# Performance work log

Measured on AMD Instinct MI355X. Metric: run time of the kernel, lower is better.

The kernel has to match this reference:

```python
import jax, jax.numpy as jnp
import numpy as np

N_Q = 9      # qubits -> state dim 512
N_L = 10     # circuit layers
DIM = 2 ** N_Q
B = 16384    # batch
N_CLS = 10


def _apply_1q(psi, U, q):
    # psi: [B, 2,...,2] (N_Q qubit axes); U: [2,2] complex
    psi = jnp.moveaxis(psi, q + 1, 1)
    shp = psi.shape
    psi = jnp.einsum('ij,bjk->bik', U, psi.reshape(shp[0], 2, -1)).reshape(shp)
    return jnp.moveaxis(psi, 1, q + 1)


def _apply_2q(psi, U, q0, q1):
    # U: [4,4] complex acting on (q0, q1)
    psi = jnp.moveaxis(psi, (q0 + 1, q1 + 1), (1, 2))
    shp = psi.shape
    psi = jnp.einsum('ij,bjk->bik', U, psi.reshape(shp[0], 4, -1)).reshape(shp)
    return jnp.moveaxis(psi, (1, 2), (q0 + 1, q1 + 1))


def _rot_mat(phi, theta, omega):
    # PennyLane Rot = RZ(omega) RY(theta) RZ(phi)
    c, s = jnp.cos(theta / 2), jnp.sin(theta / 2)
    a, b = (phi + omega) / 2, (phi - omega) / 2
    return jnp.stack([
        jnp.stack([jnp.exp(-1j * a) * c, -jnp.exp(1j * b) * s]),
        jnp.stack([jnp.exp(-1j * b) * s, jnp.exp(1j * a) * c]),
    ]).astype(jnp.complex64)


def _crx_mat(t):
    c, s = jnp.cos(t / 2), jnp.sin(t / 2)
    rx = jnp.stack([jnp.stack([c + 0j, -1j * s]),
                    jnp.stack([-1j * s, c + 0j])]).astype(jnp.complex64)
    return jnp.eye(4, dtype=jnp.complex64).at[2:, 2:].set(rx)


def _layer(psi, rot_n, crx_n):
    for i in range(N_Q):
        psi = _apply_1q(psi, _rot_mat(rot_n[i, 0], rot_n[i, 1], rot_n[i, 2]), i)
    for i in range(N_Q):
        psi = _apply_2q(psi, _crx_mat(crx_n[i, 0]), i, (i + 1) % N_Q)
    return psi


def _circuit(x, rot, crx):
    # AmplitudeEmbedding(normalize=True)
    psi = (x / jnp.linalg.norm(x, axis=1, keepdims=True)).astype(jnp.complex64)
    psi = psi.reshape((x.shape[0],) + (2,) * N_Q)
    for n in range(N_L):
        psi = _layer(psi, rot[n], crx[n])
    probs = psi.real ** 2 + psi.imag ** 2
    # <Z_q> = P(bit_q = 0) - P(bit_q = 1)
    zs = []
    for q in range(N_Q):
        axes = tuple(a for a in range(1, N_Q + 1) if a != q + 1)
        p = probs.sum(axis=axes)  # [B, 2]
        zs.append(p[:, 0] - p[:, 1])
    return jnp.stack(zs, axis=1)  # [B, N_Q]


def setup_inputs() -> dict:
    key = jax.random.key(0)
    k0, k1, k2, k3, k4 = jax.random.split(key, 5)
    x = jax.random.normal(k0, (B, DIM), jnp.float32)
    rot = jax.random.normal(k1, (N_L, N_Q, 3), jnp.float32)
    crx = jax.random.normal(k2, (N_L, N_Q, 1), jnp.float32)
    fc_w = jax.random.normal(k3, (N_CLS, N_Q), jnp.float32) * 0.3
    fc_b = jax.random.normal(k4, (N_CLS,), jnp.float32) * 0.1
    return {"x": x, "rot": rot, "crx": crx, "fc_w": fc_w, "fc_b": fc_b}


def reference(x, rot, crx, fc_w, fc_b):
    z = _circuit(x, rot, crx)          # [B, 9]
    logits = z @ fc_w.T + fc_b         # [B, 10]
    return jax.nn.log_softmax(logits, axis=1)
```

## Files before the change

kernel.cpp:

```cpp
#include <hip/hip_runtime.h>
#include <hip/hip_bf16.h>
#include <math.h>

#define NQ 9
#define NL 10
#define DIM 512
#define NCLS 10
#define B_TOT 16384

#define A_OFF   ((size_t)0)
#define BT_OFF  ((size_t)16 << 20)
#define C_OFF   ((size_t)32 << 20)
#define WS_NEED (((size_t)96) << 20)

__device__ __forceinline__ float shx(float v, int m) { return __shfl_xor(v, m, 64); }

__device__ __forceinline__ int looks_bf16(const void* p, int count) {
  const unsigned short* u = (const unsigned short*)p;
  int n = count < 64 ? count : 64;
  int good = 0;
  for (int i = 0; i < n; ++i) {
    unsigned short v = u[i];
    int e = (v >> 7) & 0xFF;
    good += (e >= 100 && e <= 140) || ((v & 0x7FFF) == 0);
  }
  return good * 8 >= n * 7;
}

__device__ __forceinline__ float ld(const void* p, int i, int isbf) {
  if (isbf) return __uint_as_float(((unsigned)((const unsigned short*)p)[i]) << 16);
  return ((const float*)p)[i];
}

template<int M>
__device__ __forceinline__ void rot_x(float (&sr)[8], float (&si)[8], const float* u) {
  float4 uA = *(const float4*)u;
  float4 uB = *(const float4*)(u + 4);
  bool hi = (threadIdx.x & M) != 0;
  float ar = hi ? uB.z : uA.x, ai = hi ? uB.w : uA.y;
  float br = hi ? uB.x : uA.z, bi = hi ? uB.y : uA.w;
#pragma unroll
  for (int r = 0; r < 8; ++r) {
    float pr = shx(sr[r], M), pi = shx(si[r], M);
    float nr = ar * sr[r] - ai * si[r] + br * pr - bi * pi;
    float ni = ar * si[r] + ai * sr[r] + br * pi + bi * pr;
    sr[r] = nr; si[r] = ni;
  }
}
template<int S>
__device__ __forceinline__ void rot_r(float (&sr)[8], float (&si)[8], const float* u) {
  float4 uA = *(const float4*)u;
  float4 uB = *(const float4*)(u + 4);
#pragma unroll
  for (int r0 = 0; r0 < 8; ++r0) {
    if (r0 & S) continue;
    int r1 = r0 + S;
    float a0r = sr[r0], a0i = si[r0], a1r = sr[r1], a1i = si[r1];
    sr[r0] = uA.x * a0r - uA.y * a0i + uA.z * a1r - uA.w * a1i;
    si[r0] = uA.x * a0i + uA.y * a0r + uA.z * a1i + uA.w * a1r;
    sr[r1] = uB.x * a0r - uB.y * a0i + uB.z * a1r - uB.w * a1i;
    si[r1] = uB.x * a0i + uB.y * a0r + uB.z * a1i + uB.w * a1r;
  }
}
template<int MC, int MT>
__device__ __forceinline__ void crx_ll(float (&sr)[8], float (&si)[8], const float* cs) {
  bool ctrl = (threadIdx.x & MC) != 0;
  float c = ctrl ? cs[0] : 1.0f;
  float s = ctrl ? cs[1] : 0.0f;
#pragma unroll
  for (int r = 0; r < 8; ++r) {
    float pr = shx(sr[r], MT), pi = shx(si[r], MT);
    float nr = c * sr[r] + s * pi;
    float ni = c * si[r] - s * pr;
    sr[r] = nr; si[r] = ni;
  }
}
template<int MC, int ST>
__device__ __forceinline__ void crx_lr(float (&sr)[8], float (&si)[8], const float* cs) {
  bool ctrl = (threadIdx.x & MC) != 0;
  float c = ctrl ? cs[0] : 1.0f;
  float s = ctrl ? cs[1] : 0.0f;
#pragma unroll
  for (int r0 = 0; r0 < 8; ++r0) {
    if (r0 & ST) continue;
    int r1 = r0 + ST;
    float a0r = sr[r0], a0i = si[r0], a1r = sr[r1], a1i = si[r1];
    sr[r0] = c * a0r + s * a1i;  si[r0] = c * a0i - s * a1r;
    sr[r1] = c * a1r + s * a0i;  si[r1] = c * a1i - s * a0r;
  }
}
template<int PC, int ST>
__device__ __forceinline__ void crx_rr(float (&sr)[8], float (&si)[8], const float* cs) {
  float c = cs[0], s = cs[1];
#pragma unroll
  for (int r0 = 0; r0 < 8; ++r0) {
    if (r0 & ST) continue;
    if (!((r0 >> PC) & 1)) continue;
    int r1 = r0 + ST;
    float a0r = sr[r0], a0i = si[r0], a1r = sr[r1], a1i = si[r1];
    sr[r0] = c * a0r + s * a1i;  si[r0] = c * a0i - s * a1r;
    sr[r1] = c * a1r + s * a0i;  si[r1] = c * a1i - s * a0r;
  }
}
template<int PC, int MT>
__device__ __forceinline__ void crx_rl(float (&sr)[8], float (&si)[8], const float* cs) {
  float c = cs[0], s = cs[1];
#pragma unroll
  for (int r = 0; r < 8; ++r) {
    if (!((r >> PC) & 1)) continue;
    float pr = shx(sr[r], MT), pi = shx(si[r], MT);
    float nr = c * sr[r] + s * pi;
    float ni = c * si[r] - s * pr;
    sr[r] = nr; si[r] = ni;
  }
}

__device__ __forceinline__ void build_gates(const void* rot, const void* crx,
                                            float* gU, float* gCS) {
  int tid = threadIdx.x;
  __shared__ int gflags[2];
  if (tid == 0) {
    gflags[0] = looks_bf16(rot, NL * NQ * 3);
    gflags[1] = looks_bf16(crx, NL * NQ);
  }
  __syncthreads();
  if (tid < NL * NQ) {
    int frot = gflags[0], fcrx = gflags[1];
    float phi = ld(rot, tid * 3 + 0, frot);
    float th  = ld(rot, tid * 3 + 1, frot);
    float om  = ld(rot, tid * 3 + 2, frot);
    float c = cosf(0.5f * th), s = sinf(0.5f * th);
    float a = 0.5f * (phi + om), b = 0.5f * (phi - om);
    float ca = cosf(a), sa = sinf(a), cb = cosf(b), sb = sinf(b);
    float* u = gU + tid * 8;
    u[0] =  ca * c; u[1] = -sa * c;
    u[2] = -cb * s; u[3] = -sb * s;
    u[4] =  cb * s; u[5] = -sb * s;
    u[6] =  ca * c; u[7] =  sa * c;
    float t2 = 0.5f * ld(crx, tid, fcrx);
    gCS[tid * 2 + 0] = cosf(t2);
    gCS[tid * 2 + 1] = sinf(t2);
  }
  __syncthreads();
}

__device__ __forceinline__ void run_circuit(float (&sr)[8], float (&si)[8],
                                            const float* gU, const float* gCS) {
#pragma unroll 1
  for (int n = 0; n < NL; ++n) {
    const float* U  = gU  + n * NQ * 8;
    const float* CS = gCS + n * NQ * 2;
    rot_x<32>(sr, si, U + 0 * 8);
    rot_x<16>(sr, si, U + 1 * 8);
    rot_x< 8>(sr, si, U + 2 * 8);
    rot_x< 4>(sr, si, U + 3 * 8);
    rot_x< 2>(sr, si, U + 4 * 8);
    rot_x< 1>(sr, si, U + 5 * 8);
    rot_r< 4>(sr, si, U + 6 * 8);
    rot_r< 2>(sr, si, U + 7 * 8);
    rot_r< 1>(sr, si, U + 8 * 8);
    crx_ll<32, 16>(sr, si, CS + 0 * 2);
    crx_ll<16,  8>(sr, si, CS + 1 * 2);
    crx_ll< 8,  4>(sr, si, CS + 2 * 2);
    crx_ll< 4,  2>(sr, si, CS + 3 * 2);
    crx_ll< 2,  1>(sr, si, CS + 4 * 2);
    crx_lr< 1,  4>(sr, si, CS + 5 * 2);
    crx_rr< 2,  2>(sr, si, CS + 6 * 2);
    crx_rr< 1,  1>(sr, si, CS + 7 * 2);
    crx_rl< 0, 32>(sr, si, CS + 8 * 2);
  }
}

template<int M>
__device__ __forceinline__ void rot_lane2(float (&sr)[2], float (&si)[2], const float* u) {
  float4 uA = *(const float4*)u;
  float4 uB = *(const float4*)(u + 4);
  bool hi = (threadIdx.x & M) != 0;
  float ar = hi ? uB.z : uA.x, ai = hi ? uB.w : uA.y;
  float br = hi ? uB.x : uA.z, bi = hi ? uB.y : uA.w;
#pragma unroll
  for (int r = 0; r < 2; ++r) {
    float pr = shx(sr[r], M), pi = shx(si[r], M);
    float nr = ar * sr[r] - ai * si[r] + br * pr - bi * pi;
    float ni = ar * si[r] + ai * sr[r] + br * pi + bi * pr;
    sr[r] = nr; si[r] = ni;
  }
}
__device__ __forceinline__ void rot_reg2(float (&sr)[2], float (&si)[2], const float* u) {
  float4 uA = *(const float4*)u;
  float4 uB = *(const float4*)(u + 4);
  float a0r = sr[0], a0i = si[0], a1r = sr[1], a1i = si[1];
  sr[0] = uA.x * a0r - uA.y * a0i + uA.z * a1r - uA.w * a1i;
  si[0] = uA.x * a0i + uA.y * a0r + uA.z * a1i + uA.w * a1r;
  sr[1] = uB.x * a0r - uB.y * a0i + uB.z * a1r - uB.w * a1i;
  si[1] = uB.x * a0i + uB.y * a0r + uB.z * a1i + uB.w * a1r;
}
__device__ __forceinline__ void crx_lane2(float (&sr)[2], float (&si)[2],
                                          float c, float s, int MT) {
#pragma unroll
  for (int r = 0; r < 2; ++r) {
    float pr = shx(sr[r], MT), pi = shx(si[r], MT);
    float nr = c * sr[r] + s * pi;
    float ni = c * si[r] - s * pr;
    sr[r] = nr; si[r] = ni;
  }
}
__device__ __forceinline__ void crx_reg2(float (&sr)[2], float (&si)[2], float c, float s) {
  float a0r = sr[0], a0i = si[0], a1r = sr[1], a1i = si[1];
  sr[0] = c * a0r + s * a1i;  si[0] = c * a0i - s * a1r;
  sr[1] = c * a1r + s * a0i;  si[1] = c * a1i - s * a0r;
}

__global__ __launch_bounds__(256) void prep_kernel(const void* __restrict__ x,
                                                   const void* __restrict__ rot,
                                                   const void* __restrict__ crx,
                                                   __hip_bfloat16* __restrict__ A,
                                                   __hip_bfloat16* __restrict__ BT) {
  int tid = threadIdx.x;
  if (blockIdx.x < DIM) {
    __shared__ __align__(16) float gU[NL * NQ * 8];
    __shared__ __align__(16) float gCS[NL * NQ * 2];
    __shared__ float sRe[DIM], sIm[DIM];
    build_gates(rot, crx, gU, gCS);
    int lane = tid & 63, wv = tid >> 6;
    int idx0 = wv * 128 + lane * 2;
    int k = blockIdx.x;
    float sr[2], si[2];
    sr[0] = (idx0 == k) ? 1.f : 0.f;
    sr[1] = (idx0 + 1 == k) ? 1.f : 0.f;
    si[0] = si[1] = 0.f;
#pragma unroll 1
    for (int n = 0; n < NL; ++n) {
      const float* U  = gU  + n * NQ * 8;
      const float* CS = gCS + n * NQ * 2;
      __syncthreads();
      sRe[idx0] = sr[0]; sIm[idx0] = si[0];
      sRe[idx0 + 1] = sr[1]; sIm[idx0 + 1] = si[1];
      __syncthreads();
      {
        const float* U0 = U; const float* U1 = U + 8;
        int a = wv >> 1, b = wv & 1;
        float mr[4], mi[4];
#pragma unroll
        for (int w2 = 0; w2 < 4; ++w2) {
          int a2 = w2 >> 1, b2 = w2 & 1;
          float u0r = U0[(a * 2 + a2) * 2], u0i = U0[(a * 2 + a2) * 2 + 1];
          float u1r = U1[(b * 2 + b2) * 2], u1i = U1[(b * 2 + b2) * 2 + 1];
          mr[w2] = u0r * u1r - u0i * u1i;
          mi[w2] = u0r * u1i + u0i * u1r;
        }
#pragma unroll
        for (int r = 0; r < 2; ++r) {
          float nr = 0.f, ni = 0.f;
#pragma unroll
          for (int w2 = 0; w2 < 4; ++w2) {
            float xr = sRe[w2 * 128 + lane * 2 + r];
            float xi = sIm[w2 * 128 + lane * 2 + r];
            nr += mr[w2] * xr - mi[w2] * xi;
            ni += mr[w2] * xi + mi[w2] * xr;
          }
          sr[r] = nr; si[r] = ni;
        }
      }
      rot_lane2<32>(sr, si, U + 2 * 8);
      rot_lane2<16>(sr, si, U + 3 * 8);
      rot_lane2< 8>(sr, si, U + 4 * 8);
      rot_lane2< 4>(sr, si, U + 5 * 8);
      rot_lane2< 2>(sr, si, U + 6 * 8);
      rot_lane2< 1>(sr, si, U + 7 * 8);
      rot_reg2(sr, si, U + 8 * 8);
      __syncthreads();
      sRe[idx0] = sr[0]; sIm[idx0] = si[0];
      sRe[idx0 + 1] = sr[1]; sIm[idx0 + 1] = si[1];
      __syncthreads();
      {
        float c = (wv & 2) ? CS[0] : 1.f, s = (wv & 2) ? CS[1] : 0.f;
        int p0 = (wv ^ 1) * 128 + lane * 2;
#pragma unroll
        for (int r = 0; r < 2; ++r) {
          float pr = sRe[p0 + r], pi = sIm[p0 + r];
          float nr = c * sr[r] + s * pi;
          float ni = c * si[r] - s * pr;
          sr[r] = nr; si[r] = ni;
        }
      }
      { float c = (wv & 1) ? CS[2] : 1.f, s = (wv & 1) ? CS[3] : 0.f;
        crx_lane2(sr, si, c, s, 32); }
      { bool ct = (lane & 32); crx_lane2(sr, si, ct ? CS[4] : 1.f, ct ? CS[5] : 0.f, 16); }
      { bool ct = (lane & 16); crx_lane2(sr, si, ct ? CS[6] : 1.f, ct ? CS[7] : 0.f, 8); }
      { bool ct = (lane &  8); crx_lane2(sr, si, ct ? CS[8] : 1.f, ct ? CS[9] : 0.f, 4); }
      { bool ct = (lane &  4); crx_lane2(sr, si, ct ? CS[10] : 1.f, ct ? CS[11] : 0.f, 2); }
      { bool ct = (lane &  2); crx_lane2(sr, si, ct ? CS[12] : 1.f, ct ? CS[13] : 0.f, 1); }
      { bool ct = (lane & 1); crx_reg2(sr, si, ct ? CS[14] : 1.f, ct ? CS[15] : 0.f); }
      __syncthreads();
      sRe[idx0] = sr[0]; sIm[idx0] = si[0];
      sRe[idx0 + 1] = sr[1]; sIm[idx0 + 1] = si[1];
      __syncthreads();
      {
        float c = CS[16], s = CS[17];
        int p1 = (wv ^ 2) * 128 + lane * 2 + 1;
        float pr = sRe[p1], pi = sIm[p1];
        float nr = c * sr[1] + s * pi;
        float ni = c * si[1] - s * pr;
        sr[1] = nr; si[1] = ni;
      }
    }
#pragma unroll
    for (int r = 0; r < 2; ++r) {
      int j = idx0 + r;
      BT[(size_t)j * DIM + k]         = __float2bfloat16(sr[r]);
      BT[(size_t)(DIM + j) * DIM + k] = __float2bfloat16(si[r]);
    }
  } else {
    __shared__ int fx;
    if (tid == 0) fx = looks_bf16(x, B_TOT * DIM);
    __syncthreads();
    size_t i0 = ((size_t)(blockIdx.x - DIM) * 256 + tid) * 8;
    if (fx) {
      *(uint4*)(A + i0) = *(const uint4*)((const unsigned short*)x + i0);
    } else {
      const float4* src = (const float4*)((const float*)x + i0);
      float4 a = src[0], b = src[1];
      __hip_bfloat16 o[8];
      o[0] = __float2bfloat16(a.x); o[1] = __float2bfloat16(a.y);
      o[2] = __float2bfloat16(a.z); o[3] = __float2bfloat16(a.w);
      o[4] = __float2bfloat16(b.x); o[5] = __float2bfloat16(b.y);
      o[6] = __float2bfloat16(b.z); o[7] = __float2bfloat16(b.w);
      *(uint4*)(A + i0) = *(uint4*)o;
    }
  }
}

using frag8 = __attribute__((ext_vector_type(8))) short;
using frag4 = __attribute__((ext_vector_type(4))) float;

typedef __attribute__((address_space(1))) const unsigned int GU32;
typedef __attribute__((address_space(3))) unsigned int LU32;
__device__ __forceinline__ void async16(const void* g, void* l) {
  __builtin_amdgcn_global_load_lds((GU32*)g, (LU32*)l, 16, 0, 0);
}

__global__ __launch_bounds__(256) void gemm_kernel(const unsigned short* __restrict__ A,
                                                   const unsigned short* __restrict__ BT,
                                                   unsigned short* __restrict__ C) {
  __shared__ __align__(16) unsigned short lA[128 * 32];
  __shared__ __align__(16) unsigned short lB[128 * 32];
  int bid = blockIdx.x;
  int xcd = bid & 7;
  int slot = bid >> 3;
  int n0 = (slot & 7) * 128;
  int m0 = (xcd * 16 + (slot >> 3)) * 128;
  int tid = threadIdx.x;
  int wv = tid >> 6, lane = tid & 63;
  int wm = wv >> 1, wn = wv & 1;
  int row = lane & 15, quad = lane >> 4;
  int srow = wv * 32 + (lane >> 2);
  int scol = (lane & 3) * 8;
  const unsigned short* gA = A + (size_t)(m0 + srow) * 512 + scol;
  const unsigned short* gB = BT + (size_t)(n0 + srow) * 512 + scol;
  frag4 acc[4][4] = {};
#pragma unroll 1
  for (int k0 = 0; k0 < 512; k0 += 32) {
    __syncthreads();
    async16(gA + k0,            &lA[(wv * 32) * 32]);
    async16(gA + k0 + 16 * 512, &lA[(wv * 32 + 16) * 32]);
    async16(gB + k0,            &lB[(wv * 32) * 32]);
    async16(gB + k0 + 16 * 512, &lB[(wv * 32 + 16) * 32]);
    __syncthreads();
    frag8 af[4], bf[4];
#pragma unroll
    for (int i = 0; i < 4; ++i) {
      af[i] = *(const frag8*)(&lA[(wm * 64 + i * 16 + row) * 32 + quad * 8]);
      bf[i] = *(const frag8*)(&lB[(wn * 64 + i * 16 + row) * 32 + quad * 8]);
    }
#pragma unroll
    for (int mi = 0; mi < 4; ++mi)
#pragma unroll
      for (int ni = 0; ni < 4; ++ni)
        acc[mi][ni] = __builtin_amdgcn_mfma_f32_16x16x32_bf16(af[mi], bf[ni],
                                                              acc[mi][ni], 0, 0, 0);
  }
#pragma unroll
  for (int mi = 0; mi < 4; ++mi)
#pragma unroll
    for (int ni = 0; ni < 4; ++ni)
#pragma unroll
      for (int rg = 0; rg < 4; ++rg) {
        int m = m0 + wm * 64 + mi * 16 + quad * 4 + rg;
        int n = n0 + wn * 64 + ni * 16 + row;
        __hip_bfloat16 h = __float2bfloat16(acc[mi][ni][rg]);
        C[(size_t)m * 1024 + n] = *(unsigned short*)&h;
      }
}

__global__ __launch_bounds__(256) void epi_kernel(const unsigned short* __restrict__ C,
                                                  const void* __restrict__ fcw,
                                                  const void* __restrict__ fcb,
                                                  float* __restrict__ out) {
  __shared__ int flags[2];
  __shared__ float sW[NCLS * NQ];
  __shared__ float sB[NCLS];
  int tid = threadIdx.x;
  if (tid == 0) {
    flags[0] = looks_bf16(fcw, NCLS * NQ);
    flags[1] = looks_bf16(fcb, NCLS);
  }
  __syncthreads();
  if (tid < NCLS * NQ) sW[tid] = ld(fcw, tid, flags[0]);
  if (tid < NCLS)      sB[tid] = ld(fcb, tid, flags[1]);
  __syncthreads();
  int b = (blockIdx.x * 256 + tid) >> 6;
  int lane = tid & 63;
  const unsigned short* rowp = C + (size_t)b * 1024;
  const uint4 ur = *(const uint4*)(rowp + lane * 8);
  const uint4 ui = *(const uint4*)(rowp + 512 + lane * 8);
  float cr[8], ci[8];
  cr[0] = __uint_as_float(ur.x << 16); cr[1] = __uint_as_float(ur.x & 0xffff0000u);
  cr[2] = __uint_as_float(ur.y << 16); cr[3] = __uint_as_float(ur.y & 0xffff0000u);
  cr[4] = __uint_as_float(ur.z << 16); cr[5] = __uint_as_float(ur.z & 0xffff0000u);
  cr[6] = __uint_as_float(ur.w << 16); cr[7] = __uint_as_float(ur.w & 0xffff0000u);
  ci[0] = __uint_as_float(ui.x << 16); ci[1] = __uint_as_float(ui.x & 0xffff0000u);
  ci[2] = __uint_as_float(ui.y << 16); ci[3] = __uint_as_float(ui.y & 0xffff0000u);
  ci[4] = __uint_as_float(ui.z << 16); ci[5] = __uint_as_float(ui.z & 0xffff0000u);
  ci[6] = __uint_as_float(ui.w << 16); ci[7] = __uint_as_float(ui.w & 0xffff0000u);
  float p[8], P = 0.f;
#pragma unroll
  for (int r = 0; r < 8; ++r) { p[r] = cr[r] * cr[r] + ci[r] * ci[r]; P += p[r]; }
  float z[NQ + 1];
#pragma unroll
  for (int q = 0; q < 6; ++q) z[q] = (lane & (32 >> q)) ? -P : P;
  z[6] = z[7] = z[8] = 0.f;
#pragma unroll
  for (int r = 0; r < 8; ++r) {
    z[6] += (r & 4) ? -p[r] : p[r];
    z[7] += (r & 2) ? -p[r] : p[r];
    z[8] += (r & 1) ? -p[r] : p[r];
  }
  z[9] = P;
#pragma unroll
  for (int m = 1; m < 64; m <<= 1) {
#pragma unroll
    for (int q = 0; q < NQ + 1; ++q) z[q] += shx(z[q], m);
  }
  float invP = 1.0f / z[9];
#pragma unroll
  for (int q = 0; q < NQ; ++q) z[q] *= invP;
  float lg[NCLS], mx = -1e30f;
#pragma unroll
  for (int k = 0; k < NCLS; ++k) {
    float t = sB[k];
#pragma unroll
    for (int q = 0; q < NQ; ++q) t += z[q] * sW[k * NQ + q];
    lg[k] = t; mx = fmaxf(mx, t);
  }
  float se = 0.f;
#pragma unroll
  for (int k = 0; k < NCLS; ++k) se += expf(lg[k] - mx);
  float lse = mx + logf(se);
  if (lane < NCLS) out[(size_t)b * NCLS + lane] = lg[lane] - lse;
}

__global__ __launch_bounds__(256) void qnn_kernel(
    const void* __restrict__ x, const void* __restrict__ rot,
    const void* __restrict__ crx, const void* __restrict__ fcw,
    const void* __restrict__ fcb, float* __restrict__ out) {
  __shared__ __align__(16) float gU[NL * NQ * 8];
  __shared__ __align__(16) float gCS[NL * NQ * 2];
  __shared__ int flags[3];
  int tid = threadIdx.x;
  if (tid == 0) {
    flags[0] = looks_bf16(x, B_TOT * DIM);
    flags[1] = looks_bf16(fcw, NCLS * NQ);
    flags[2] = looks_bf16(fcb, NCLS);
  }
  build_gates(rot, crx, gU, gCS);
  __syncthreads();
  int wid = (blockIdx.x * blockDim.x + tid) >> 6;
  int lane = tid & 63;
  float sr[8], si[8];
  if (flags[0]) {
    const uint4 u = *(const uint4*)((const unsigned short*)x + (size_t)wid * DIM + lane * 8);
    sr[0] = __uint_as_float(u.x << 16); sr[1] = __uint_as_float(u.x & 0xffff0000u);
    sr[2] = __uint_as_float(u.y << 16); sr[3] = __uint_as_float(u.y & 0xffff0000u);
    sr[4] = __uint_as_float(u.z << 16); sr[5] = __uint_as_float(u.z & 0xffff0000u);
    sr[6] = __uint_as_float(u.w << 16); sr[7] = __uint_as_float(u.w & 0xffff0000u);
  } else {
    const float4* xf = (const float4*)((const float*)x + (size_t)wid * DIM) + lane * 2;
    float4 a = xf[0], b = xf[1];
    sr[0] = a.x; sr[1] = a.y; sr[2] = a.z; sr[3] = a.w;
    sr[4] = b.x; sr[5] = b.y; sr[6] = b.z; sr[7] = b.w;
  }
  float nrm = 0.f;
#pragma unroll
  for (int r = 0; r < 8; ++r) { nrm += sr[r] * sr[r]; si[r] = 0.f; }
#pragma unroll
  for (int m = 1; m < 64; m <<= 1) nrm += shx(nrm, m);
  float inv = rsqrtf(nrm);
  inv = inv * (1.5f - 0.5f * nrm * inv * inv);
#pragma unroll
  for (int r = 0; r < 8; ++r) sr[r] *= inv;
  run_circuit(sr, si, gU, gCS);
  float p[8], P = 0.f;
#pragma unroll
  for (int r = 0; r < 8; ++r) { p[r] = sr[r] * sr[r] + si[r] * si[r]; P += p[r]; }
  float z[NQ];
#pragma unroll
  for (int q = 0; q < 6; ++q) z[q] = (lane & (32 >> q)) ? -P : P;
  z[6] = z[7] = z[8] = 0.f;
#pragma unroll
  for (int r = 0; r < 8; ++r) {
    z[6] += (r & 4) ? -p[r] : p[r];
    z[7] += (r & 2) ? -p[r] : p[r];
    z[8] += (r & 1) ? -p[r] : p[r];
  }
#pragma unroll
  for (int m = 1; m < 64; m <<= 1) {
#pragma unroll
    for (int q = 0; q < NQ; ++q) z[q] += shx(z[q], m);
  }
  int ffw = flags[1], ffb = flags[2];
  float lg[NCLS], mx = -1e30f;
#pragma unroll
  for (int k = 0; k < NCLS; ++k) {
    float t = ld(fcb, k, ffb);
#pragma unroll
    for (int q = 0; q < NQ; ++q) t += z[q] * ld(fcw, k * NQ + q, ffw);
    lg[k] = t; mx = fmaxf(mx, t);
  }
  float se = 0.f;
#pragma unroll
  for (int k = 0; k < NCLS; ++k) se += expf(lg[k] - mx);
  float lse = mx + logf(se);
  if (lane < NCLS) out[(size_t)wid * NCLS + lane] = lg[lane] - lse;
}

extern "C" void kernel_launch(void* const* d_in, const int* in_sizes, int n_in,
                              void* d_out, int out_size, void* d_ws, size_t ws_size,
                              hipStream_t stream) {
  const void* x   = d_in[0];
  const void* rot = d_in[1];
  const void* crx = d_in[2];
  const void* fcw = d_in[3];
  const void* fcb = d_in[4];
  float* out = (float*)d_out;
  if (ws_size >= WS_NEED) {
    __hip_bfloat16* A  = (__hip_bfloat16*)((char*)d_ws + A_OFF);
    __hip_bfloat16* BT = (__hip_bfloat16*)((char*)d_ws + BT_OFF);
    unsigned short* C  = (unsigned short*)((char*)d_ws + C_OFF);
    prep_kernel<<<DIM + (B_TOT * DIM) / (256 * 8), 256, 0, stream>>>(x, rot, crx, A, BT);
    gemm_kernel<<<(B_TOT / 128) * (1024 / 128), 256, 0, stream>>>(
        (const unsigned short*)A, (const unsigned short*)BT, C);
    epi_kernel<<<(B_TOT * 64) / 256, 256, 0, stream>>>(C, fcw, fcb, out);
  } else {
    qnn_kernel<<<(B_TOT * 64) / 256, 256, 0, stream>>>(x, rot, crx, fcw, fcb, out);
  }
}
```

Before: 165.2 us.

## Fuse probability and Z-expectation reduction into GEMM epilogue, write per-panel partials

The GEMM epilogue now squares each output amplitude, applies sign masks per qubit and reduces across lanes and warps through shared memory. It writes 10 partial sums per row per column panel instead of storing the full bf16 state matrix. A small reduction kernel sums the 8 panels and applies the linear layer and log-softmax. This removes the write and re-read of the 32 MB intermediate C, at the cost of more epilogue ALU work and shuffles inside the GEMM.

```diff
diff --git a/kernel.cpp b/kernel.cpp
--- a/kernel.cpp
+++ b/kernel.cpp
@@ -10,7 +10,7 @@
 
 #define A_OFF   ((size_t)0)
 #define BT_OFF  ((size_t)16 << 20)
-#define C_OFF   ((size_t)32 << 20)
+#define ZP_OFF  ((size_t)32 << 20)
 #define WS_NEED (((size_t)96) << 20)
 
 __device__ __forceinline__ float shx(float v, int m) { return __shfl_xor(v, m, 64); }
@@ -340,11 +340,12 @@
   __builtin_amdgcn_global_load_lds((GU32*)g, (LU32*)l, 16, 0, 0);
 }
 
-__global__ __launch_bounds__(256) void gemm_kernel(const unsigned short* __restrict__ A,
-                                                   const unsigned short* __restrict__ BT,
-                                                   unsigned short* __restrict__ C) {
-  __shared__ __align__(16) unsigned short lA[128 * 32];
-  __shared__ __align__(16) unsigned short lB[128 * 32];
+__global__ __launch_bounds__(256) void gemm_z_kernel(const unsigned short* __restrict__ A,
+                                                     const unsigned short* __restrict__ BT,
+                                                     float* __restrict__ Zp) {
+  __shared__ __align__(16) unsigned short lsm[2 * 128 * 32];
+  unsigned short* lA = lsm;
+  unsigned short* lB = lsm + 128 * 32;
   int bid = blockIdx.x;
   int xcd = bid & 7;
   int slot = bid >> 3;
@@ -380,23 +381,62 @@
         acc[mi][ni] = __builtin_amdgcn_mfma_f32_16x16x32_bf16(af[mi], bf[ni],
                                                               acc[mi][ni], 0, 0, 0);
   }
-#pragma unroll
-  for (int mi = 0; mi < 4; ++mi)
-#pragma unroll
-    for (int ni = 0; ni < 4; ++ni)
+  float* zbuf = (float*)lsm;
+  __syncthreads();
+  for (int i = tid; i < 2 * 128 * 10; i += 256) zbuf[i] = 0.f;
+  __syncthreads();
+  int colbase = n0 + wn * 64 + (lane & 15);
+#pragma unroll 1
+  for (int mi = 0; mi < 4; ++mi) {
+    float zacc[4][10];
+#pragma unroll
+    for (int rg = 0; rg < 4; ++rg)
+#pragma unroll
+      for (int q = 0; q < 10; ++q) zacc[rg][q] = 0.f;
+#pragma unroll
+    for (int ni = 0; ni < 4; ++ni) {
+      int j = (colbase + ni * 16) & 511;
+      float sg[9];
+#pragma unroll
+      for (int q = 0; q < 9; ++q)
+        sg[q] = ((j >> (8 - q)) & 1) ? -1.f : 1.f;
 #pragma unroll
       for (int rg = 0; rg < 4; ++rg) {
-        int m = m0 + wm * 64 + mi * 16 + quad * 4 + rg;
-        int n = n0 + wn * 64 + ni * 16 + row;
-        __hip_bfloat16 h = __float2bfloat16(acc[mi][ni][rg]);
-        C[(size_t)m * 1024 + n] = *(unsigned short*)&h;
+        float v = acc[mi][ni][rg];
+        float p = v * v;
+#pragma unroll
+        for (int q = 0; q < 9; ++q) zacc[rg][q] += sg[q] * p;
+        zacc[rg][9] += p;
       }
-}
-
-__global__ __launch_bounds__(256) void epi_kernel(const unsigned short* __restrict__ C,
-                                                  const void* __restrict__ fcw,
-                                                  const void* __restrict__ fcb,
-                                                  float* __restrict__ out) {
+    }
+#pragma unroll
+    for (int m = 1; m < 16; m <<= 1)
+#pragma unroll
+      for (int rg = 0; rg < 4; ++rg)
+#pragma unroll
+        for (int q = 0; q < 10; ++q) zacc[rg][q] += shx(zacc[rg][q], m);
+    if ((lane & 15) == 0) {
+      int rowl = wm * 64 + mi * 16 + quad * 4;
+#pragma unroll
+      for (int rg = 0; rg < 4; ++rg)
+#pragma unroll
+        for (int q = 0; q < 10; ++q)
+          zbuf[(wn * 128 + rowl + rg) * 10 + q] = zacc[rg][q];
+    }
+  }
+  __syncthreads();
+  int panel = n0 >> 7;
+  for (int i = tid; i < 128 * 10; i += 256) {
+    int rowl = i / 10, q = i - rowl * 10;
+    float v = zbuf[rowl * 10 + q] + zbuf[(128 + rowl) * 10 + q];
+    Zp[(size_t)panel * (B_TOT * 10) + (size_t)(m0 + rowl) * 10 + q] = v;
+  }
+}
+
+__global__ __launch_bounds__(256) void zred_kernel(const float* __restrict__ Zp,
+                                                   const void* __restrict__ fcw,
+                                                   const void* __restrict__ fcb,
+                                                   float* __restrict__ out) {
   __shared__ int flags[2];
   __shared__ float sW[NCLS * NQ];
   __shared__ float sB[NCLS];
@@ -409,38 +449,15 @@
   if (tid < NCLS * NQ) sW[tid] = ld(fcw, tid, flags[0]);
   if (tid < NCLS)      sB[tid] = ld(fcb, tid, flags[1]);
   __syncthreads();
-  int b = (blockIdx.x * 256 + tid) >> 6;
-  int lane = tid & 63;
-  const unsigned short* rowp = C + (size_t)b * 1024;
-  const uint4 ur = *(const uint4*)(rowp + lane * 8);
-  const uint4 ui = *(const uint4*)(rowp + 512 + lane * 8);
-  float cr[8], ci[8];
-  cr[0] = __uint_as_float(ur.x << 16); cr[1] = __uint_as_float(ur.x & 0xffff0000u);
-  cr[2] = __uint_as_float(ur.y << 16); cr[3] = __uint_as_float(ur.y & 0xffff0000u);
-  cr[4] = __uint_as_float(ur.z << 16); cr[5] = __uint_as_float(ur.z & 0xffff0000u);
-  cr[6] = __uint_as_float(ur.w << 16); cr[7] = __uint_as_float(ur.w & 0xffff0000u);
-  ci[0] = __uint_as_float(ui.x << 16); ci[1] = __uint_as_float(ui.x & 0xffff0000u);
-  ci[2] = __uint_as_float(ui.y << 16); ci[3] = __uint_as_float(ui.y & 0xffff0000u);
-  ci[4] = __uint_as_float(ui.z << 16); ci[5] = __uint_as_float(ui.z & 0xffff0000u);
-  ci[6] = __uint_as_float(ui.w << 16); ci[7] = __uint_as_float(ui.w & 0xffff0000u);
-  float p[8], P = 0.f;
-#pragma unroll
-  for (int r = 0; r < 8; ++r) { p[r] = cr[r] * cr[r] + ci[r] * ci[r]; P += p[r]; }
-  float z[NQ + 1];
-#pragma unroll
-  for (int q = 0; q < 6; ++q) z[q] = (lane & (32 >> q)) ? -P : P;
-  z[6] = z[7] = z[8] = 0.f;
-#pragma unroll
-  for (int r = 0; r < 8; ++r) {
-    z[6] += (r & 4) ? -p[r] : p[r];
-    z[7] += (r & 2) ? -p[r] : p[r];
-    z[8] += (r & 1) ? -p[r] : p[r];
-  }
-  z[9] = P;
-#pragma unroll
-  for (int m = 1; m < 64; m <<= 1) {
-#pragma unroll
-    for (int q = 0; q < NQ + 1; ++q) z[q] += shx(z[q], m);
+  int row = blockIdx.x * 256 + tid;
+  float z[10];
+#pragma unroll
+  for (int q = 0; q < 10; ++q) z[q] = 0.f;
+#pragma unroll
+  for (int pnl = 0; pnl < 8; ++pnl) {
+    const float* p = Zp + (size_t)pnl * (B_TOT * 10) + (size_t)row * 10;
+#pragma unroll
+    for (int q = 0; q < 10; ++q) z[q] += p[q];
   }
   float invP = 1.0f / z[9];
 #pragma unroll
@@ -457,7 +474,8 @@
 #pragma unroll
   for (int k = 0; k < NCLS; ++k) se += expf(lg[k] - mx);
   float lse = mx + logf(se);
-  if (lane < NCLS) out[(size_t)b * NCLS + lane] = lg[lane] - lse;
+#pragma unroll
+  for (int k = 0; k < NCLS; ++k) out[(size_t)row * NCLS + k] = lg[k] - lse;
 }
 
 __global__ __launch_bounds__(256) void qnn_kernel(
@@ -546,11 +564,11 @@
   if (ws_size >= WS_NEED) {
     __hip_bfloat16* A  = (__hip_bfloat16*)((char*)d_ws + A_OFF);
     __hip_bfloat16* BT = (__hip_bfloat16*)((char*)d_ws + BT_OFF);
-    unsigned short* C  = (unsigned short*)((char*)d_ws + C_OFF);
+    float*          Zp = (float*)((char*)d_ws + ZP_OFF);
     prep_kernel<<<DIM + (B_TOT * DIM) / (256 * 8), 256, 0, stream>>>(x, rot, crx, A, BT);
-    gemm_kernel<<<(B_TOT / 128) * (1024 / 128), 256, 0, stream>>>(
-        (const unsigned short*)A, (const unsigned short*)BT, C);
-    epi_kernel<<<(B_TOT * 64) / 256, 256, 0, stream>>>(C, fcw, fcb, out);
+    gemm_z_kernel<<<(B_TOT / 128) * (1024 / 128), 256, 0, stream>>>(
+        (const unsigned short*)A, (const unsigned short*)BT, Zp);
+    zred_kernel<<<B_TOT / 256, 256, 0, stream>>>(Zp, fcw, fcb, out);
   } else {
     qnn_kernel<<<(B_TOT * 64) / 256, 256, 0, stream>>>(x, rot, crx, fcw, fcb, out);
   }
```

Result: slower. 457.7 us (+177.1%).
